# Optimization experiments

Measured on AMD Instinct MI355X. Metric: run time of the kernel, lower is better.

## Reference

```python
import jax, jax.numpy as jnp
import numpy as np

E = 16        # n_experts
N = 4         # n_mhc
D = 512       # d_hidden
D_FFN = int(D * 1.618)  # 828
TOP_PROB = 0.8
MAX_K = 4
SINKHORN_ITERS = 6
EPS = 1e-8


def top_prob_max_k(logits, threshold=TOP_PROB, max_k=MAX_K):
    probs = jax.nn.softmax(logits, axis=-1)
    order = jnp.argsort(-probs, axis=-1)                       # descending sort indices
    sorted_p = jnp.take_along_axis(probs, order, axis=-1)
    cumsum = jnp.cumsum(sorted_p, axis=-1)
    ar = jnp.arange(logits.shape[-1])
    mask = (cumsum - sorted_p < threshold) & (ar < max_k)
    mask = mask.at[..., 0].set(True)
    selected = sorted_p * mask.astype(probs.dtype)
    inv = jnp.argsort(order, axis=-1)                          # inverse permutation == scatter
    return jnp.take_along_axis(selected, inv, axis=-1)


def sinkhorn_knopp(M, n_iters=SINKHORN_ITERS):
    M = jnp.exp(M)
    for _ in range(n_iters):
        M = M / M.sum(axis=-1, keepdims=True)
        M = M / M.sum(axis=-2, keepdims=True)
    return M


def setup_inputs() -> dict:
    key = jax.random.key(0)
    ks = jax.random.split(key, 12)
    nd = N * D
    inp = {
        'stream': jax.random.normal(ks[0], (2, N, 1024, D), dtype=jnp.float32),
        # BatchedMHC params
        'norm_w': jnp.ones((E, nd), dtype=jnp.float32),
        'phi_pre_w': jax.random.normal(ks[1], (E, N, nd), dtype=jnp.float32) * 0.01,
        'phi_post_w': jax.random.normal(ks[2], (E, N, nd), dtype=jnp.float32) * 0.01,
        'phi_res_w': jax.random.normal(ks[3], (E, N * N, nd), dtype=jnp.float32) * 0.01,
        'b_pre': jnp.zeros((E, N), dtype=jnp.float32),
        'b_post': jnp.zeros((E, N), dtype=jnp.float32),
        'b_res': jnp.zeros((E, N, N), dtype=jnp.float32),
        'alpha_pre': jnp.ones((E,), dtype=jnp.float32),
        'alpha_post': jnp.ones((E,), dtype=jnp.float32),
        'alpha_res': jnp.ones((E,), dtype=jnp.float32),
        # SwiGLU expert params
        'swiglu_norm_w': jnp.ones((E, D), dtype=jnp.float32),
        'swiglu_wd_w': jax.random.normal(ks[4], (E, D, D), dtype=jnp.float32) * 0.01,
        'swiglu_wu_w': jax.random.normal(ks[5], (E, D, D), dtype=jnp.float32) * 0.01,
        'swiglu_gate_w': jax.random.normal(ks[6], (E, D_FFN, D), dtype=jnp.float32) * 0.01,
        'swiglu_up_w': jax.random.normal(ks[7], (E, D_FFN, D), dtype=jnp.float32) * 0.01,
        'swiglu_down_w': jax.random.normal(ks[8], (E, D, D_FFN), dtype=jnp.float32) * 0.01,
        # router (nn.Linear without bias): logits = x @ W.T, W: (E, D)
        'router_w': jax.random.normal(ks[9], (E, D), dtype=jnp.float32) * (1.0 / np.sqrt(D)),
    }
    return inp


def reference(stream, norm_w, phi_pre_w, phi_post_w, phi_res_w,
              b_pre, b_post, b_res, alpha_pre, alpha_post, alpha_res,
              swiglu_norm_w, swiglu_wd_w, swiglu_wu_w,
              swiglu_gate_w, swiglu_up_w, swiglu_down_w, router_w):
    B, n, T, d = stream.shape
    nd = n * d

    # ---- routing (eval mode: no gumbel) ----
    route_input = stream.mean(axis=1)                               # (B,T,d)
    router_logits = jnp.einsum('btd,ed->bte', route_input, router_w)
    gate_moe = top_prob_max_k(router_logits)                        # (B,T,E)
    router_probs = jax.nn.softmax(router_logits, axis=-1)
    moe_mask = (gate_moe > 0).astype(router_probs.dtype)
    route_lp = (jnp.maximum(jnp.log(router_probs), -10.0) * moe_mask).sum(-1)  # (B,T)

    # Original gathers active experts (always excluding expert 0) and skips gate==0
    # experts; since gate_e multiplies each expert's output, computing all experts
    # 1..E-1 is mathematically identical. K = E-1.
    sl = slice(1, E)

    # ---- BatchedMHC ----
    x = stream.transpose(0, 2, 1, 3).reshape(B, T, nd)              # (B,T,nd)
    rms = jax.lax.rsqrt(jnp.mean(x * x, axis=-1, keepdims=True) + EPS)
    xn = x * rms                                                    # (B,T,nd)
    # fold per-expert norm weight into the phi projections (avoids K*B*T*nd tensor)
    phi_pre_eff = phi_pre_w[sl] * norm_w[sl, None, :]               # (K,n,nd)
    phi_post_eff = phi_post_w[sl] * norm_w[sl, None, :]
    phi_res_eff = phi_res_w[sl] * norm_w[sl, None, :]               # (K,n*n,nd)

    H_pre = jax.nn.sigmoid(alpha_pre[sl, None, None, None]
                           * jnp.einsum('btd,knd->kbtn', xn, phi_pre_eff)
                           + b_pre[sl, None, None, :])              # (K,B,T,n)
    H_post = 2.0 * jax.nn.sigmoid(alpha_post[sl, None, None, None]
                                  * jnp.einsum('btd,knd->kbtn', xn, phi_post_eff)
                                  + b_post[sl, None, None, :])      # (K,B,T,n)
    res_e = jnp.einsum('btd,knd->kbtn', xn, phi_res_eff)
    K = E - 1
    H_res_raw = (alpha_res[sl].reshape(K, 1, 1, 1, 1)
                 * res_e.reshape(K, B, T, n, n)
                 + b_res[sl, None, None, :, :])
    H_res = sinkhorn_knopp(H_res_raw)                               # (K,B,T,n,n)

    # ---- per-expert SwiGLU ----
    h_e = jnp.einsum('kbtn,bntd->kbtd', H_pre, stream)              # (K,B,T,d)
    rms2 = jax.lax.rsqrt(jnp.mean(h_e * h_e, axis=-1, keepdims=True) + EPS)
    h = h_e * rms2 * swiglu_norm_w[sl, None, None, :]

    wd_out = jnp.einsum('kbtd,kod->kbto', h, swiglu_wd_w[sl])
    g = jax.nn.sigmoid(jnp.einsum('kbtd,kod->kbto', jax.nn.silu(wd_out), swiglu_wu_w[sl]))
    gate_out = jnp.einsum('kbtd,kod->kbto', h, swiglu_gate_w[sl])   # (K,B,T,d_ffn)
    up_out = jnp.einsum('kbtd,kod->kbto', h, swiglu_up_w[sl])
    out_e = g * jnp.einsum('kbtf,kof->kbto', jax.nn.silu(gate_out) * up_out,
                           swiglu_down_w[sl])                        # (K,B,T,d)

    # ---- combine ----
    gate_4d = gate_moe[:, :, 1:].transpose(2, 0, 1)[:, :, None, :, None]  # (K,B,1,T,1)
    res = jnp.einsum('kbtij,bjtd->kbitd', H_res, stream)            # (K,B,n,T,d)
    post = jnp.einsum('kbtn,kbtd->kbntd', H_post, out_e)            # (K,B,n,T,d)
    stream_update = (gate_4d * (res + post)).sum(axis=0)            # (B,n,T,d)

    return stream_update, gate_moe, route_lp
```

## Files before the change

### kernel.cpp

```cpp
#include <hip/hip_runtime.h>
#include <hip/hip_bf16.h>
#include <math.h>

typedef __attribute__((ext_vector_type(8))) short short8;
typedef __attribute__((ext_vector_type(4))) float floatx4;

#define T_LEN 1024
#define D_H 512
#define ND 2048
#define KEXP 15
#define DFFN 828
#define DFFN_P 896
#define BT_TOT 2048
#define PHI_ROWS 360
#define PHI_ROWS_P 384
#define PAIR_CAP 9216

#define WD_OFF   0
#define WU_OFF   262144
#define GATE_OFF 524288
#define UP_OFF   983040
#define DOWN_OFF 1441792
#define EXPW     1900544

#define BK 32

__device__ __forceinline__ float sigmoidf_(float x) { return 1.f / (1.f + expf(-x)); }
__device__ __forceinline__ unsigned short bf16b_(float x) {
    __hip_bfloat16 h = __float2bfloat16(x);
    return *reinterpret_cast<unsigned short*>(&h);
}

__device__ __forceinline__ void gload16(const __hip_bfloat16* g, unsigned short* l) {
    __builtin_amdgcn_global_load_lds(
        (const __attribute__((address_space(1))) void*)(uintptr_t)g,
        (__attribute__((address_space(3))) void*)(unsigned int)(uintptr_t)l,
        16, 0, 0);
}

__global__ __launch_bounds__(64) void router_kernel(
    const float* __restrict__ stream, const float* __restrict__ rw,
    float* __restrict__ gate_out, float* __restrict__ lp_out,
    int* __restrict__ cnt, int* __restrict__ list, int* __restrict__ pos)
{
    int bt = blockIdx.x; int b = bt >> 10; int t = bt & 1023;
    int lane = threadIdx.x;
    float ri[8];
#pragma unroll
    for (int w = 0; w < 8; ++w) {
        int d = lane + w * 64;
        float s = 0.f;
#pragma unroll
        for (int n = 0; n < 4; ++n)
            s += stream[(((size_t)b * 4 + n) * T_LEN + t) * D_H + d];
        ri[w] = 0.25f * s;
    }
    float logits[16];
    for (int e = 0; e < 16; ++e) {
        float p = 0.f;
#pragma unroll
        for (int w = 0; w < 8; ++w) p += ri[w] * rw[e * D_H + lane + w * 64];
#pragma unroll
        for (int off = 32; off; off >>= 1) p += __shfl_xor(p, off, 64);
        logits[e] = p;
    }
    float mx = logits[0];
    for (int e = 1; e < 16; ++e) mx = fmaxf(mx, logits[e]);
    float pr[16]; float sum = 0.f;
    for (int e = 0; e < 16; ++e) { pr[e] = expf(logits[e] - mx); sum += pr[e]; }
    float inv = 1.f / sum;
    for (int e = 0; e < 16; ++e) pr[e] *= inv;

    float gate[16]; bool taken[16];
    for (int e = 0; e < 16; ++e) { gate[e] = 0.f; taken[e] = false; }
    float prefix = 0.f;
    for (int rank = 0; rank < 4; ++rank) {
        int best = -1; float bp = -1.f;
        for (int e = 0; e < 16; ++e)
            if (!taken[e] && pr[e] > bp) { bp = pr[e]; best = e; }
        taken[best] = true;
        bool sel = (rank == 0) || (prefix < 0.8f);
        if (sel) gate[best] = bp;
        prefix += bp;
        if (!sel) break;
    }
    float lp = 0.f;
    for (int e = 0; e < 16; ++e)
        if (gate[e] > 0.f) lp += fmaxf(logf(pr[e]), -10.f);
    if (lane < 16) gate_out[(size_t)bt * 16 + lane] = gate[lane];
    if (lane == 0) lp_out[bt] = lp;
    if (lane >= 1 && lane < 16 && gate[lane] > 0.f) {
        int k = lane - 1;
        int p = atomicAdd(&cnt[k], 1);
        list[k * BT_TOT + p] = bt;
        pos[k * BT_TOT + bt] = p;
    }
}

__global__ void scan_kernel(const int* __restrict__ cnt, int* __restrict__ offs) {
    if (threadIdx.x == 0) {
        int a = 0;
        for (int k = 0; k < KEXP; ++k) { offs[k] = a; a += (cnt[k] + 63) & ~63; }
        offs[KEXP] = a;
    }
}

__global__ __launch_bounds__(256) void xn_kernel(
    const float* __restrict__ stream, __hip_bfloat16* __restrict__ xn)
{
    int bt = blockIdx.x; int b = bt >> 10; int t = bt & 1023;
    int tid = threadIdx.x;
    float v[8]; float ss = 0.f;
#pragma unroll
    for (int w = 0; w < 8; ++w) {
        int j = tid + w * 256;
        int n = j >> 9, d = j & 511;
        float x = stream[(((size_t)b * 4 + n) * T_LEN + t) * D_H + d];
        v[w] = x; ss += x * x;
    }
#pragma unroll
    for (int off = 32; off; off >>= 1) ss += __shfl_down(ss, off, 64);
    __shared__ float red[4];
    int wave = tid >> 6, lane = tid & 63;
    if (lane == 0) red[wave] = ss;
    __syncthreads();
    float tot = red[0] + red[1] + red[2] + red[3];
    float r = rsqrtf(tot / (float)ND + 1e-8f);
#pragma unroll
    for (int w = 0; w < 8; ++w)
        xn[(size_t)bt * ND + tid + w * 256] = __float2bfloat16(v[w] * r);
}

__global__ __launch_bounds__(256) void cvt_phi_kernel(
    const float* __restrict__ norm_w, const float* __restrict__ phi_pre,
    const float* __restrict__ phi_post, const float* __restrict__ phi_res,
    __hip_bfloat16* __restrict__ phi_all)
{
    int idx = blockIdx.x * 256 + threadIdx.x;
    int row = idx >> 11, col = idx & 2047;
    float v = 0.f;
    if (row < PHI_ROWS) {
        int k = row / 24, j = row - k * 24, e = k + 1;
        float nw = norm_w[(size_t)e * ND + col];
        float p;
        if (j < 4)      p = phi_pre[((size_t)e * 4 + j) * ND + col];
        else if (j < 8) p = phi_post[((size_t)e * 4 + (j - 4)) * ND + col];
        else            p = phi_res[((size_t)e * 16 + (j - 8)) * ND + col];
        v = p * nw;
    }
    phi_all[idx] = __float2bfloat16(v);
}

__global__ __launch_bounds__(256) void cvt_all_kernel(
    const float* __restrict__ wd, const float* __restrict__ wu,
    const float* __restrict__ gate, const float* __restrict__ up,
    const float* __restrict__ down, __hip_bfloat16* __restrict__ wbuf, int e0)
{
    int z = blockIdx.z;
    int type = blockIdx.y;
    int g = blockIdx.x * 256 + threadIdx.x;
    int e = e0 + z;
    __hip_bfloat16* dstb = wbuf + (size_t)z * EXPW;
    float4 v = make_float4(0.f, 0.f, 0.f, 0.f);
    size_t didx;
    if (type <= 1) {
        if (g >= 65536) return;
        didx = (type == 0 ? WD_OFF : WU_OFF) + (size_t)g * 4;
        const float* src = (type == 0 ? wd : wu) + (size_t)e * 262144;
        v = *(const float4*)(src + (size_t)g * 4);
    } else if (type <= 3) {
        if (g >= 114688) return;
        size_t idx4 = (size_t)g * 4;
        didx = (type == 2 ? GATE_OFF : UP_OFF) + idx4;
        if (idx4 < (size_t)DFFN * 512) {
            const float* src = (type == 2 ? gate : up) + (size_t)e * DFFN * 512;
            v = *(const float4*)(src + idx4);
        }
    } else {
        if (g >= 114688) return;
        int r = g / 224, gc = g - r * 224;
        didx = DOWN_OFF + (size_t)g * 4;
        if (gc < 207)
            v = *(const float4*)(down + (size_t)e * 512 * DFFN + (size_t)r * DFFN + gc * 4);
    }
    ushort4 o;
    o.x = bf16b_(v.x); o.y = bf16b_(v.y); o.z = bf16b_(v.z); o.w = bf16b_(v.w);
    *(ushort4*)((unsigned short*)dstb + didx) = o;
}

#define LDSS 40
__global__ __launch_bounds__(256) void gemm_dense(
    const __hip_bfloat16* __restrict__ A, const __hip_bfloat16* __restrict__ W,
    float* __restrict__ Cf, int Ka, int Oc, int kLen, int kzStride)
{
    __shared__ __align__(16) unsigned short As[128 * LDSS];
    __shared__ __align__(16) unsigned short Ws[128 * LDSS];
    int z = blockIdx.z;
    int bo = blockIdx.x * 128;
    int bm = blockIdx.y * 128;
    int kbeg = z * kzStride;
    int tid = threadIdx.x;
    int wid = tid >> 6, lane = tid & 63;
    int quad = lane >> 4, lr = lane & 15;
    int wm = (wid & 1) * 64, wn = (wid >> 1) * 64;
    int srow = tid >> 2;
    int schk = (tid & 3) * 8;

    floatx4 acc[4][4];
#pragma unroll
    for (int i = 0; i < 4; ++i)
#pragma unroll
        for (int j = 0; j < 4; ++j) { floatx4 zv = {0.f, 0.f, 0.f, 0.f}; acc[i][j] = zv; }

    for (int k0 = kbeg; k0 < kbeg + kLen; k0 += BK) {
        float4 a0 = *(const float4*)(A + (size_t)(bm + srow) * Ka + k0 + schk);
        float4 a1 = *(const float4*)(A + (size_t)(bm + srow + 64) * Ka + k0 + schk);
        float4 w0 = *(const float4*)(W + (size_t)(bo + srow) * Ka + k0 + schk);
        float4 w1 = *(const float4*)(W + (size_t)(bo + srow + 64) * Ka + k0 + schk);
        __syncthreads();
        *(float4*)&As[srow * LDSS + schk] = a0;
        *(float4*)&As[(srow + 64) * LDSS + schk] = a1;
        *(float4*)&Ws[srow * LDSS + schk] = w0;
        *(float4*)&Ws[(srow + 64) * LDSS + schk] = w1;
        __syncthreads();
        short8 af[4], bf[4];
#pragma unroll
        for (int mi = 0; mi < 4; ++mi)
            af[mi] = *(const short8*)&As[(wm + mi * 16 + lr) * LDSS + quad * 8];
#pragma unroll
        for (int ni = 0; ni < 4; ++ni)
            bf[ni] = *(const short8*)&Ws[(wn + ni * 16 + lr) * LDSS + quad * 8];
#pragma unroll
        for (int mi = 0; mi < 4; ++mi)
#pragma unroll
            for (int ni = 0; ni < 4; ++ni)
                acc[mi][ni] = __builtin_amdgcn_mfma_f32_16x16x32_bf16(
                    af[mi], bf[ni], acc[mi][ni], 0, 0, 0);
    }
#pragma unroll
    for (int mi = 0; mi < 4; ++mi) {
        int row0 = bm + wm + mi * 16 + quad * 4;
#pragma unroll
        for (int ni = 0; ni < 4; ++ni) {
            int col = bo + wn + ni * 16 + lr;
#pragma unroll
            for (int r = 0; r < 4; ++r)
                atomicAdd(&Cf[(size_t)(row0 + r) * Oc + col], acc[mi][ni][r]);
        }
    }
}

__global__ __launch_bounds__(256) void gemm_stage1(
    const __hip_bfloat16* __restrict__ hA, const __hip_bfloat16* __restrict__ wbuf,
    __hip_bfloat16* __restrict__ s1A, __hip_bfloat16* __restrict__ tA,
    const int* __restrict__ cnt, const int* __restrict__ offs, int kg)
{
    __shared__ __align__(16) unsigned short As[64 * 32];
    __shared__ __align__(16) unsigned short Gs[128 * 32];
    __shared__ __align__(16) unsigned short Us[128 * 32];
    int z = blockIdx.z;
    int k = kg + z;
    int bm = blockIdx.y * 64;
    if (bm >= cnt[k]) return;
    int base = offs[k];
    bool dual = (blockIdx.x >= 4);
    int bo = (dual ? (blockIdx.x - 4) : blockIdx.x) * 128;
    const __hip_bfloat16* Ab = hA + (size_t)base * D_H;
    const __hip_bfloat16* W1 = wbuf + (size_t)z * EXPW + (dual ? GATE_OFF : WD_OFF);
    const __hip_bfloat16* W2 = wbuf + (size_t)z * EXPW + UP_OFF;
    int tid = threadIdx.x;
    int wid = tid >> 6, lane = tid & 63;
    int quad = lane >> 4, lr = lane & 15;
    int lrow = lane >> 2, lchk = lane & 3;
    int achk = lchk ^ ((lrow >> 1) & 3);
    int fs = quad ^ ((lr >> 1) & 3);
    int wm = (wid & 1) * 32, wn = (wid >> 1) * 64;

    floatx4 a1[2][4], a2[2][4];
#pragma unroll
    for (int i = 0; i < 2; ++i)
#pragma unroll
        for (int j = 0; j < 4; ++j) {
            floatx4 zv = {0.f, 0.f, 0.f, 0.f};
            a1[i][j] = zv; a2[i][j] = zv;
        }

    int sr0 = wid * 16 + lrow;
    int sr1 = (wid + 4) * 16 + lrow;
    const size_t aoff  = (size_t)(bm + sr0) * D_H + achk * 8;
    const size_t g0off = (size_t)(bo + sr0) * D_H + achk * 8;
    const size_t g1off = (size_t)(bo + sr1) * D_H + achk * 8;

    for (int k0 = 0; k0 < D_H; k0 += BK) {
        __syncthreads();
        gload16(Ab + aoff + k0, As + wid * 512);
        gload16(W1 + g0off + k0, Gs + wid * 512);
        gload16(W1 + g1off + k0, Gs + (wid + 4) * 512);
        if (dual) {
            gload16(W2 + g0off + k0, Us + wid * 512);
            gload16(W2 + g1off + k0, Us + (wid + 4) * 512);
        }
        __syncthreads();
        short8 af[2], bg[4];
#pragma unroll
        for (int mi = 0; mi < 2; ++mi)
            af[mi] = *(const short8*)&As[(wm + mi * 16 + lr) * 32 + fs * 8];
#pragma unroll
        for (int ni = 0; ni < 4; ++ni)
            bg[ni] = *(const short8*)&Gs[(wn + ni * 16 + lr) * 32 + fs * 8];
#pragma unroll
        for (int mi = 0; mi < 2; ++mi)
#pragma unroll
            for (int ni = 0; ni < 4; ++ni)
                a1[mi][ni] = __builtin_amdgcn_mfma_f32_16x16x32_bf16(
                    af[mi], bg[ni], a1[mi][ni], 0, 0, 0);
        if (dual) {
            short8 bu[4];
#pragma unroll
            for (int ni = 0; ni < 4; ++ni)
                bu[ni] = *(const short8*)&Us[(wn + ni * 16 + lr) * 32 + fs * 8];
#pragma unroll
            for (int mi = 0; mi < 2; ++mi)
#pragma unroll
                for (int ni = 0; ni < 4; ++ni)
                    a2[mi][ni] = __builtin_amdgcn_mfma_f32_16x16x32_bf16(
                        af[mi], bu[ni], a2[mi][ni], 0, 0, 0);
        }
    }

#pragma unroll
    for (int mi = 0; mi < 2; ++mi) {
        int row0 = bm + wm + mi * 16 + quad * 4;
#pragma unroll
        for (int ni = 0; ni < 4; ++ni) {
            int col = bo + wn + ni * 16 + lr;
#pragma unroll
            for (int r = 0; r < 4; ++r) {
                float v = a1[mi][ni][r];
                if (dual) {
                    float uu = a2[mi][ni][r];
                    tA[(size_t)(base + row0 + r) * DFFN_P + col] =
                        __float2bfloat16(v * sigmoidf_(v) * uu);
                } else {
                    s1A[(size_t)(base + row0 + r) * D_H + col] =
                        __float2bfloat16(v * sigmoidf_(v));
                }
            }
        }
    }
}

__global__ __launch_bounds__(256) void gemm_final(
    const __hip_bfloat16* __restrict__ s1A, const __hip_bfloat16* __restrict__ tA,
    const __hip_bfloat16* __restrict__ wbuf, __hip_bfloat16* __restrict__ outeA,
    const int* __restrict__ cnt, const int* __restrict__ offs, int kg)
{
    __shared__ __align__(16) unsigned short As[64 * 32];
    __shared__ __align__(16) unsigned short Ws[128 * 32];
    int z = blockIdx.z;
    int k = kg + z;
    int bm = blockIdx.y * 64;
    if (bm >= cnt[k]) return;
    int base = offs[k];
    int bo = blockIdx.x * 128;
    const __hip_bfloat16* A1 = s1A + (size_t)base * D_H;
    const __hip_bfloat16* A2 = tA + (size_t)base * DFFN_P;
    const __hip_bfloat16* Wu = wbuf + (size_t)z * EXPW + WU_OFF;
    const __hip_bfloat16* Wd = wbuf + (size_t)z * EXPW + DOWN_OFF;
    int tid = threadIdx.x;
    int wid = tid >> 6, lane = tid & 63;
    int quad = lane >> 4, lr = lane & 15;
    int lrow = lane >> 2, lchk = lane & 3;
    int achk = lchk ^ ((lrow >> 1) & 3);
    int fs = quad ^ ((lr >> 1) & 3);
    int wm = (wid & 1) * 32, wn = (wid >> 1) * 64;
    int sr0 = wid * 16 + lrow;
    int sr1 = (wid + 4) * 16 + lrow;

    floatx4 accg[2][4], accd[2][4];
#pragma unroll
    for (int i = 0; i < 2; ++i)
#pragma unroll
        for (int j = 0; j < 4; ++j) {
            floatx4 zv = {0.f, 0.f, 0.f, 0.f};
            accg[i][j] = zv; accd[i][j] = zv;
        }

    for (int k0 = 0; k0 < D_H; k0 += BK) {
        __syncthreads();
        gload16(A1 + (size_t)(bm + sr0) * D_H + k0 + achk * 8, As + wid * 512);
        gload16(Wu + (size_t)(bo + sr0) * D_H + k0 + achk * 8, Ws + wid * 512);
        gload16(Wu + (size_t)(bo + sr1) * D_H + k0 + achk * 8, Ws + (wid + 4) * 512);
        __syncthreads();
        short8 af[2], bf[4];
#pragma unroll
        for (int mi = 0; mi < 2; ++mi)
            af[mi] = *(const short8*)&As[(wm + mi * 16 + lr) * 32 + fs * 8];
#pragma unroll
        for (int ni = 0; ni < 4; ++ni)
            bf[ni] = *(const short8*)&Ws[(wn + ni * 16 + lr) * 32 + fs * 8];
#pragma unroll
        for (int mi = 0; mi < 2; ++mi)
#pragma unroll
            for (int ni = 0; ni < 4; ++ni)
                accg[mi][ni] = __builtin_amdgcn_mfma_f32_16x16x32_bf16(
                    af[mi], bf[ni], accg[mi][ni], 0, 0, 0);
    }
    for (int k0 = 0; k0 < DFFN_P; k0 += BK) {
        __syncthreads();
        gload16(A2 + (size_t)(bm + sr0) * DFFN_P + k0 + achk * 8, As + wid * 512);
        gload16(Wd + (size_t)(bo + sr0) * DFFN_P + k0 + achk * 8, Ws + wid * 512);
        gload16(Wd + (size_t)(bo + sr1) * DFFN_P + k0 + achk * 8, Ws + (wid + 4) * 512);
        __syncthreads();
        short8 af[2], bf[4];
#pragma unroll
        for (int mi = 0; mi < 2; ++mi)
            af[mi] = *(const short8*)&As[(wm + mi * 16 + lr) * 32 + fs * 8];
#pragma unroll
        for (int ni = 0; ni < 4; ++ni)
            bf[ni] = *(const short8*)&Ws[(wn + ni * 16 + lr) * 32 + fs * 8];
#pragma unroll
        for (int mi = 0; mi < 2; ++mi)
#pragma unroll
            for (int ni = 0; ni < 4; ++ni)
                accd[mi][ni] = __builtin_amdgcn_mfma_f32_16x16x32_bf16(
                    af[mi], bf[ni], accd[mi][ni], 0, 0, 0);
    }

#pragma unroll
    for (int mi = 0; mi < 2; ++mi) {
        int row0 = bm + wm + mi * 16 + quad * 4;
#pragma unroll
        for (int ni = 0; ni < 4; ++ni) {
            int col = bo + wn + ni * 16 + lr;
#pragma unroll
            for (int r = 0; r < 4; ++r) {
                float g = accg[mi][ni][r];
                float d = accd[mi][ni][r];
                outeA[(size_t)(base + row0 + r) * D_H + col] =
                    __float2bfloat16(sigmoidf_(g) * d);
            }
        }
    }
}

__global__ __launch_bounds__(256) void mhc_post_kernel(
    const float* __restrict__ Cproj,
    const float* __restrict__ b_pre, const float* __restrict__ b_post,
    const float* __restrict__ b_res, const float* __restrict__ a_pre,
    const float* __restrict__ a_post, const float* __restrict__ a_res,
    float* __restrict__ Hpre, float* __restrict__ Hpost, float* __restrict__ Hres)
{
    int gid = blockIdx.x * 256 + threadIdx.x;
    int k = gid >> 11, bt = gid & 2047, e = k + 1;
    const float* s = Cproj + (size_t)bt * PHI_ROWS_P + k * 24;
    float ap = a_pre[e], aq = a_post[e], ar = a_res[e];
#pragma unroll
    for (int n = 0; n < 4; ++n)
        Hpre[((size_t)k * BT_TOT + bt) * 4 + n] = sigmoidf_(ap * s[n] + b_pre[e * 4 + n]);
#pragma unroll
    for (int n = 0; n < 4; ++n)
        Hpost[((size_t)k * BT_TOT + bt) * 4 + n] = 2.f * sigmoidf_(aq * s[4 + n] + b_post[e * 4 + n]);
    float M[16];
#pragma unroll
    for (int i = 0; i < 16; ++i) M[i] = expf(ar * s[8 + i] + b_res[e * 16 + i]);
#pragma unroll
    for (int it = 0; it < 6; ++it) {
#pragma unroll
        for (int i = 0; i < 4; ++i) {
            float iv = 1.f / (M[i*4] + M[i*4+1] + M[i*4+2] + M[i*4+3]);
            M[i*4] *= iv; M[i*4+1] *= iv; M[i*4+2] *= iv; M[i*4+3] *= iv;
        }
#pragma unroll
        for (int j = 0; j < 4; ++j) {
            float iv = 1.f / (M[j] + M[4+j] + M[8+j] + M[12+j]);
            M[j] *= iv; M[4+j] *= iv; M[8+j] *= iv; M[12+j] *= iv;
        }
    }
#pragma unroll
    for (int i = 0; i < 16; ++i) Hres[((size_t)k * BT_TOT + bt) * 16 + i] = M[i];
}

__global__ __launch_bounds__(256) void h_kernel(
    const float* __restrict__ stream, const float* __restrict__ Hpre,
    const float* __restrict__ sw_norm, const int* __restrict__ list,
    const int* __restrict__ counts, const int* __restrict__ offs,
    __hip_bfloat16* __restrict__ hA)
{
    int k = blockIdx.y;
    int i = blockIdx.x;
    if (i >= counts[k]) return;
    int bt = list[k * BT_TOT + i];
    int e = k + 1;
    int b = bt >> 10, t = bt & 1023;
    int tid = threadIdx.x;
    float hp[4];
#pragma unroll
    for (int n = 0; n < 4; ++n) hp[n] = Hpre[((size_t)k * BT_TOT + bt) * 4 + n];
    float he[2]; float ss = 0.f;
#pragma unroll
    for (int w = 0; w < 2; ++w) {
        int d = tid + w * 256;
        float v = 0.f;
#pragma unroll
        for (int n = 0; n < 4; ++n)
            v += hp[n] * stream[(((size_t)b * 4 + n) * T_LEN + t) * D_H + d];
        he[w] = v; ss += v * v;
    }
#pragma unroll
    for (int off = 32; off; off >>= 1) ss += __shfl_down(ss, off, 64);
    __shared__ float red[4];
    int wave = tid >> 6, lane = tid & 63;
    if (lane == 0) red[wave] = ss;
    __syncthreads();
    float tot = red[0] + red[1] + red[2] + red[3];
    float r = rsqrtf(tot / (float)D_H + 1e-8f);
    size_t row = (size_t)(offs[k] + i);
#pragma unroll
    for (int w = 0; w < 2; ++w) {
        int d = tid + w * 256;
        hA[row * D_H + d] = __float2bfloat16(he[w] * r * sw_norm[(size_t)e * D_H + d]);
    }
}

__global__ __launch_bounds__(256) void combine_kernel(
    const float* __restrict__ stream, const __hip_bfloat16* __restrict__ outeA,
    const float* __restrict__ Hpost, const float* __restrict__ Hres,
    const float* __restrict__ gate_all, const int* __restrict__ pos,
    const int* __restrict__ offs, float* __restrict__ out)
{
    int bt = blockIdx.x; int b = bt >> 10; int t = bt & 1023;
    int tid = threadIdx.x;
    float s[2][4], accv[2][4];
#pragma unroll
    for (int w = 0; w < 2; ++w) {
        int d = tid + w * 256;
#pragma unroll
        for (int n = 0; n < 4; ++n) {
            s[w][n] = stream[(((size_t)b * 4 + n) * T_LEN + t) * D_H + d];
            accv[w][n] = 0.f;
        }
    }
    for (int k = 0; k < KEXP; ++k) {
        float gate = gate_all[(size_t)bt * 16 + k + 1];
        if (gate == 0.f) continue;
        size_t row = (size_t)(offs[k] + pos[k * BT_TOT + bt]);
        float hr[16], hp[4];
#pragma unroll
        for (int i = 0; i < 16; ++i) hr[i] = Hres[((size_t)k * BT_TOT + bt) * 16 + i];
#pragma unroll
        for (int i = 0; i < 4; ++i) hp[i] = Hpost[((size_t)k * BT_TOT + bt) * 4 + i];
#pragma unroll
        for (int w = 0; w < 2; ++w) {
            int d = tid + w * 256;
            float oe = __bfloat162float(outeA[row * D_H + d]);
#pragma unroll
            for (int i = 0; i < 4; ++i) {
                float v = hp[i] * oe + hr[i*4+0]*s[w][0] + hr[i*4+1]*s[w][1]
                        + hr[i*4+2]*s[w][2] + hr[i*4+3]*s[w][3];
                accv[w][i] += gate * v;
            }
        }
    }
#pragma unroll
    for (int w = 0; w < 2; ++w) {
        int d = tid + w * 256;
#pragma unroll
        for (int i = 0; i < 4; ++i)
            out[(((size_t)b * 4 + i) * T_LEN + t) * D_H + d] = accv[w][i];
    }
}

extern "C" void kernel_launch(void* const* d_in, const int* in_sizes, int n_in,
                              void* d_out, int out_size, void* d_ws, size_t ws_size,
                              hipStream_t stream) {
    const float* stream_in = (const float*)d_in[0];
    const float* norm_w    = (const float*)d_in[1];
    const float* phi_pre   = (const float*)d_in[2];
    const float* phi_post  = (const float*)d_in[3];
    const float* phi_res   = (const float*)d_in[4];
    const float* b_pre     = (const float*)d_in[5];
    const float* b_post    = (const float*)d_in[6];
    const float* b_res     = (const float*)d_in[7];
    const float* alpha_pre = (const float*)d_in[8];
    const float* alpha_post= (const float*)d_in[9];
    const float* alpha_res = (const float*)d_in[10];
    const float* sw_norm   = (const float*)d_in[11];
    const float* wd_w      = (const float*)d_in[12];
    const float* wu_w      = (const float*)d_in[13];
    const float* gate_w    = (const float*)d_in[14];
    const float* up_w      = (const float*)d_in[15];
    const float* down_w    = (const float*)d_in[16];
    const float* router_w  = (const float*)d_in[17];

    float* out = (float*)d_out;
    const int SU_N = 2 * 4 * T_LEN * D_H;
    float* gate_out = out + SU_N;
    float* lp_out = gate_out + BT_TOT * 16;

    char* p = (char*)d_ws;
    __hip_bfloat16* xn     = (__hip_bfloat16*)p; p += (size_t)BT_TOT * ND * 2;
    __hip_bfloat16* phiall = (__hip_bfloat16*)p; p += (size_t)PHI_ROWS_P * ND * 2;
    float* Cproj = (float*)p; p += (size_t)BT_TOT * PHI_ROWS_P * 4;
    float* Hpre  = (float*)p; p += (size_t)KEXP * BT_TOT * 4 * 4;
    float* Hpost = (float*)p; p += (size_t)KEXP * BT_TOT * 4 * 4;
    float* Hres  = (float*)p; p += (size_t)KEXP * BT_TOT * 16 * 4;
    int* cnt  = (int*)p; p += 256;
    int* offs = (int*)p; p += 256;
    int* list = (int*)p; p += (size_t)KEXP * BT_TOT * 4;
    int* pos  = (int*)p; p += (size_t)KEXP * BT_TOT * 4;
    __hip_bfloat16* hA    = (__hip_bfloat16*)p; p += (size_t)PAIR_CAP * D_H * 2;
    __hip_bfloat16* s1A   = (__hip_bfloat16*)p; p += (size_t)PAIR_CAP * D_H * 2;
    __hip_bfloat16* outeA = (__hip_bfloat16*)p; p += (size_t)PAIR_CAP * D_H * 2;
    __hip_bfloat16* tA    = (__hip_bfloat16*)p; p += (size_t)PAIR_CAP * DFFN_P * 2;
    size_t fixed_bytes = (size_t)(p - (char*)d_ws);
    size_t perW = (size_t)EXPW * 2;
    size_t avail = ws_size > fixed_bytes ? ws_size - fixed_bytes : 0;
    int G = (int)(avail / perW);
    if (G > KEXP) G = KEXP;
    if (G < 1) G = 1;
    __hip_bfloat16* wbuf = (__hip_bfloat16*)p;

    hipMemsetAsync(cnt, 0, 64, stream);
    hipMemsetAsync(Cproj, 0, (size_t)BT_TOT * PHI_ROWS_P * 4, stream);
    router_kernel<<<BT_TOT, 64, 0, stream>>>(
        stream_in, router_w, gate_out, lp_out, cnt, list, pos);
    scan_kernel<<<1, 64, 0, stream>>>(cnt, offs);
    xn_kernel<<<BT_TOT, 256, 0, stream>>>(stream_in, xn);
    cvt_phi_kernel<<<(PHI_ROWS_P * ND) / 256, 256, 0, stream>>>(
        norm_w, phi_pre, phi_post, phi_res, phiall);
    gemm_dense<<<dim3(3, 16, 4), 256, 0, stream>>>(
        xn, phiall, Cproj, ND, PHI_ROWS_P, 512, 512);
    mhc_post_kernel<<<(KEXP * BT_TOT) / 256, 256, 0, stream>>>(
        Cproj, b_pre, b_post, b_res, alpha_pre, alpha_post, alpha_res, Hpre, Hpost, Hres);
    h_kernel<<<dim3(BT_TOT, KEXP), 256, 0, stream>>>(
        stream_in, Hpre, sw_norm, list, cnt, offs, hA);

    for (int kg = 0; kg < KEXP; kg += G) {
        int Gc = (kg + G <= KEXP) ? G : (KEXP - kg);
        int e0 = kg + 1;
        cvt_all_kernel<<<dim3(448, 5, Gc), 256, 0, stream>>>(
            wd_w, wu_w, gate_w, up_w, down_w, wbuf, e0);
        gemm_stage1<<<dim3(11, 32, Gc), 256, 0, stream>>>(
            hA, wbuf, s1A, tA, cnt, offs, kg);
        gemm_final<<<dim3(4, 32, Gc), 256, 0, stream>>>(
            s1A, tA, wbuf, outeA, cnt, offs, kg);
    }

    combine_kernel<<<BT_TOT, 256, 0, stream>>>(
        stream_in, outeA, Hpost, Hres, gate_out, pos, offs, out);
}
```

Baseline: 400.3 us.

## Fuse router into RMS-norm prep, fold MHC post into h_kernel, enlarge expert GEMM M-tile

Merges the router and xn normalization kernels into one prep_kernel that reads the stream once, and moves the per-pair Sinkhorn/sigmoid MHC coefficient computation into h_kernel so the Hpre buffer and the separate mhc_post launch go away. The expert GEMMs switch to 128-row M tiles with 512 threads, halving the number of M blocks and letting each wave load one row slice. Segment padding grows to 128 and the pair capacity is raised to match. In exchange, a single thread does the routing softmax/top-k serially per block, and the Sinkhorn work now runs on one thread inside h_kernel before a block barrier.

```diff
diff --git a/kernel.cpp b/kernel.cpp
--- a/kernel.cpp
+++ b/kernel.cpp
@@ -14,7 +14,7 @@
 #define BT_TOT 2048
 #define PHI_ROWS 360
 #define PHI_ROWS_P 384
-#define PAIR_CAP 9216
+#define PAIR_CAP 10240
 
 #define WD_OFF   0
 #define WU_OFF   262144
@@ -38,78 +38,15 @@
         16, 0, 0);
 }
 
-__global__ __launch_bounds__(64) void router_kernel(
+__global__ __launch_bounds__(256) void prep_kernel(
     const float* __restrict__ stream, const float* __restrict__ rw,
-    float* __restrict__ gate_out, float* __restrict__ lp_out,
-    int* __restrict__ cnt, int* __restrict__ list, int* __restrict__ pos)
-{
-    int bt = blockIdx.x; int b = bt >> 10; int t = bt & 1023;
-    int lane = threadIdx.x;
-    float ri[8];
-#pragma unroll
-    for (int w = 0; w < 8; ++w) {
-        int d = lane + w * 64;
-        float s = 0.f;
-#pragma unroll
-        for (int n = 0; n < 4; ++n)
-            s += stream[(((size_t)b * 4 + n) * T_LEN + t) * D_H + d];
-        ri[w] = 0.25f * s;
-    }
-    float logits[16];
-    for (int e = 0; e < 16; ++e) {
-        float p = 0.f;
-#pragma unroll
-        for (int w = 0; w < 8; ++w) p += ri[w] * rw[e * D_H + lane + w * 64];
-#pragma unroll
-        for (int off = 32; off; off >>= 1) p += __shfl_xor(p, off, 64);
-        logits[e] = p;
-    }
-    float mx = logits[0];
-    for (int e = 1; e < 16; ++e) mx = fmaxf(mx, logits[e]);
-    float pr[16]; float sum = 0.f;
-    for (int e = 0; e < 16; ++e) { pr[e] = expf(logits[e] - mx); sum += pr[e]; }
-    float inv = 1.f / sum;
-    for (int e = 0; e < 16; ++e) pr[e] *= inv;
-
-    float gate[16]; bool taken[16];
-    for (int e = 0; e < 16; ++e) { gate[e] = 0.f; taken[e] = false; }
-    float prefix = 0.f;
-    for (int rank = 0; rank < 4; ++rank) {
-        int best = -1; float bp = -1.f;
-        for (int e = 0; e < 16; ++e)
-            if (!taken[e] && pr[e] > bp) { bp = pr[e]; best = e; }
-        taken[best] = true;
-        bool sel = (rank == 0) || (prefix < 0.8f);
-        if (sel) gate[best] = bp;
-        prefix += bp;
-        if (!sel) break;
-    }
-    float lp = 0.f;
-    for (int e = 0; e < 16; ++e)
-        if (gate[e] > 0.f) lp += fmaxf(logf(pr[e]), -10.f);
-    if (lane < 16) gate_out[(size_t)bt * 16 + lane] = gate[lane];
-    if (lane == 0) lp_out[bt] = lp;
-    if (lane >= 1 && lane < 16 && gate[lane] > 0.f) {
-        int k = lane - 1;
-        int p = atomicAdd(&cnt[k], 1);
-        list[k * BT_TOT + p] = bt;
-        pos[k * BT_TOT + bt] = p;
-    }
-}
-
-__global__ void scan_kernel(const int* __restrict__ cnt, int* __restrict__ offs) {
-    if (threadIdx.x == 0) {
-        int a = 0;
-        for (int k = 0; k < KEXP; ++k) { offs[k] = a; a += (cnt[k] + 63) & ~63; }
-        offs[KEXP] = a;
-    }
-}
-
-__global__ __launch_bounds__(256) void xn_kernel(
-    const float* __restrict__ stream, __hip_bfloat16* __restrict__ xn)
+    __hip_bfloat16* __restrict__ xn, float* __restrict__ gate_out,
+    float* __restrict__ lp_out, int* __restrict__ cnt,
+    int* __restrict__ list, int* __restrict__ pos)
 {
     int bt = blockIdx.x; int b = bt >> 10; int t = bt & 1023;
     int tid = threadIdx.x;
+    int wave = tid >> 6, lane = tid & 63;
     float v[8]; float ss = 0.f;
 #pragma unroll
     for (int w = 0; w < 8; ++w) {
@@ -118,17 +55,71 @@
         float x = stream[(((size_t)b * 4 + n) * T_LEN + t) * D_H + d];
         v[w] = x; ss += x * x;
     }
+    float m0 = 0.25f * (v[0] + v[2] + v[4] + v[6]);
+    float m1 = 0.25f * (v[1] + v[3] + v[5] + v[7]);
+    __shared__ float redE[4][16];
+    __shared__ float logit_s[16];
+    for (int e = 0; e < 16; ++e) {
+        float p = m0 * rw[e * D_H + tid] + m1 * rw[e * D_H + tid + 256];
+#pragma unroll
+        for (int off = 32; off; off >>= 1) p += __shfl_xor(p, off, 64);
+        if (lane == 0) redE[wave][e] = p;
+    }
 #pragma unroll
     for (int off = 32; off; off >>= 1) ss += __shfl_down(ss, off, 64);
-    __shared__ float red[4];
-    int wave = tid >> 6, lane = tid & 63;
-    if (lane == 0) red[wave] = ss;
+    __shared__ float redS[4];
+    if (lane == 0) redS[wave] = ss;
     __syncthreads();
-    float tot = red[0] + red[1] + red[2] + red[3];
+    if (tid < 16) logit_s[tid] = redE[0][tid] + redE[1][tid] + redE[2][tid] + redE[3][tid];
+    __syncthreads();
+    if (tid == 0) {
+        float pr[16];
+        float mx = logit_s[0];
+        for (int e = 1; e < 16; ++e) mx = fmaxf(mx, logit_s[e]);
+        float sum = 0.f;
+        for (int e = 0; e < 16; ++e) { pr[e] = expf(logit_s[e] - mx); sum += pr[e]; }
+        float inv = 1.f / sum;
+        for (int e = 0; e < 16; ++e) pr[e] *= inv;
+        float gate[16]; bool taken[16];
+        for (int e = 0; e < 16; ++e) { gate[e] = 0.f; taken[e] = false; }
+        float prefix = 0.f;
+        for (int rank = 0; rank < 4; ++rank) {
+            int best = -1; float bp = -1.f;
+            for (int e = 0; e < 16; ++e)
+                if (!taken[e] && pr[e] > bp) { bp = pr[e]; best = e; }
+            taken[best] = true;
+            bool sel = (rank == 0) || (prefix < 0.8f);
+            if (sel) gate[best] = bp;
+            prefix += bp;
+            if (!sel) break;
+        }
+        float lp = 0.f;
+        for (int e = 0; e < 16; ++e) {
+            gate_out[(size_t)bt * 16 + e] = gate[e];
+            if (gate[e] > 0.f) lp += fmaxf(logf(pr[e]), -10.f);
+        }
+        lp_out[bt] = lp;
+        for (int e = 1; e < 16; ++e)
+            if (gate[e] > 0.f) {
+                int k = e - 1;
+                int p = atomicAdd(&cnt[k], 1);
+                list[k * BT_TOT + p] = bt;
+                pos[k * BT_TOT + bt] = p;
+            }
+    }
+    float tot = redS[0] + redS[1] + redS[2] + redS[3];
     float r = rsqrtf(tot / (float)ND + 1e-8f);
 #pragma unroll
     for (int w = 0; w < 8; ++w)
         xn[(size_t)bt * ND + tid + w * 256] = __float2bfloat16(v[w] * r);
+}
+
+__global__ void scan_kernel(const int* __restrict__ cnt, int* __restrict__ offs) {
+    if (threadIdx.x == 0) {
+        int a = 0;
+        for (int k = 0; k < KEXP; ++k) { offs[k] = a; a += (cnt[k] + 127) & ~127; }
+        offs[KEXP] = a;
+    }
 }
 
 __global__ __launch_bounds__(256) void cvt_phi_kernel(
@@ -250,17 +241,17 @@
     }
 }
 
-__global__ __launch_bounds__(256) void gemm_stage1(
+__global__ __launch_bounds__(512) void gemm_stage1(
     const __hip_bfloat16* __restrict__ hA, const __hip_bfloat16* __restrict__ wbuf,
     __hip_bfloat16* __restrict__ s1A, __hip_bfloat16* __restrict__ tA,
     const int* __restrict__ cnt, const int* __restrict__ offs, int kg)
 {
-    __shared__ __align__(16) unsigned short As[64 * 32];
+    __shared__ __align__(16) unsigned short As[128 * 32];
     __shared__ __align__(16) unsigned short Gs[128 * 32];
     __shared__ __align__(16) unsigned short Us[128 * 32];
     int z = blockIdx.z;
     int k = kg + z;
-    int bm = blockIdx.y * 64;
+    int bm = blockIdx.y * 128;
     if (bm >= cnt[k]) return;
     int base = offs[k];
     bool dual = (blockIdx.x >= 4);
@@ -274,7 +265,9 @@
     int lrow = lane >> 2, lchk = lane & 3;
     int achk = lchk ^ ((lrow >> 1) & 3);
     int fs = quad ^ ((lr >> 1) & 3);
-    int wm = (wid & 1) * 32, wn = (wid >> 1) * 64;
+    int wm = (wid & 3) * 32, wn = (wid >> 2) * 64;
+    int srow = wid * 16 + lrow;
+    int ldsb = wid * 512;
 
     floatx4 a1[2][4], a2[2][4];
 #pragma unroll
@@ -285,21 +278,14 @@
             a1[i][j] = zv; a2[i][j] = zv;
         }
 
-    int sr0 = wid * 16 + lrow;
-    int sr1 = (wid + 4) * 16 + lrow;
-    const size_t aoff  = (size_t)(bm + sr0) * D_H + achk * 8;
-    const size_t g0off = (size_t)(bo + sr0) * D_H + achk * 8;
-    const size_t g1off = (size_t)(bo + sr1) * D_H + achk * 8;
+    const size_t aoff = (size_t)(bm + srow) * D_H + achk * 8;
+    const size_t woff = (size_t)(bo + srow) * D_H + achk * 8;
 
     for (int k0 = 0; k0 < D_H; k0 += BK) {
         __syncthreads();
-        gload16(Ab + aoff + k0, As + wid * 512);
-        gload16(W1 + g0off + k0, Gs + wid * 512);
-        gload16(W1 + g1off + k0, Gs + (wid + 4) * 512);
-        if (dual) {
-            gload16(W2 + g0off + k0, Us + wid * 512);
-            gload16(W2 + g1off + k0, Us + (wid + 4) * 512);
-        }
+        gload16(Ab + aoff + k0, As + ldsb);
+        gload16(W1 + woff + k0, Gs + ldsb);
+        if (dual) gload16(W2 + woff + k0, Us + ldsb);
         __syncthreads();
         short8 af[2], bg[4];
 #pragma unroll
@@ -350,16 +336,16 @@
     }
 }
 
-__global__ __launch_bounds__(256) void gemm_final(
+__global__ __launch_bounds__(512) void gemm_final(
     const __hip_bfloat16* __restrict__ s1A, const __hip_bfloat16* __restrict__ tA,
     const __hip_bfloat16* __restrict__ wbuf, __hip_bfloat16* __restrict__ outeA,
     const int* __restrict__ cnt, const int* __restrict__ offs, int kg)
 {
-    __shared__ __align__(16) unsigned short As[64 * 32];
+    __shared__ __align__(16) unsigned short As[128 * 32];
     __shared__ __align__(16) unsigned short Ws[128 * 32];
     int z = blockIdx.z;
     int k = kg + z;
-    int bm = blockIdx.y * 64;
+    int bm = blockIdx.y * 128;
     if (bm >= cnt[k]) return;
     int base = offs[k];
     int bo = blockIdx.x * 128;
@@ -373,9 +359,9 @@
     int lrow = lane >> 2, lchk = lane & 3;
     int achk = lchk ^ ((lrow >> 1) & 3);
     int fs = quad ^ ((lr >> 1) & 3);
-    int wm = (wid & 1) * 32, wn = (wid >> 1) * 64;
-    int sr0 = wid * 16 + lrow;
-    int sr1 = (wid + 4) * 16 + lrow;
+    int wm = (wid & 3) * 32, wn = (wid >> 2) * 64;
+    int srow = wid * 16 + lrow;
+    int ldsb = wid * 512;
 
     floatx4 accg[2][4], accd[2][4];
 #pragma unroll
@@ -388,9 +374,8 @@
 
     for (int k0 = 0; k0 < D_H; k0 += BK) {
         __syncthreads();
-        gload16(A1 + (size_t)(bm + sr0) * D_H + k0 + achk * 8, As + wid * 512);
-        gload16(Wu + (size_t)(bo + sr0) * D_H + k0 + achk * 8, Ws + wid * 512);
-        gload16(Wu + (size_t)(bo + sr1) * D_H + k0 + achk * 8, Ws + (wid + 4) * 512);
+        gload16(A1 + (size_t)(bm + srow) * D_H + k0 + achk * 8, As + ldsb);
+        gload16(Wu + (size_t)(bo + srow) * D_H + k0 + achk * 8, Ws + ldsb);
         __syncthreads();
         short8 af[2], bf[4];
 #pragma unroll
@@ -408,9 +393,8 @@
     }
     for (int k0 = 0; k0 < DFFN_P; k0 += BK) {
         __syncthreads();
-        gload16(A2 + (size_t)(bm + sr0) * DFFN_P + k0 + achk * 8, As + wid * 512);
-        gload16(Wd + (size_t)(bo + sr0) * DFFN_P + k0 + achk * 8, Ws + wid * 512);
-        gload16(Wd + (size_t)(bo + sr1) * DFFN_P + k0 + achk * 8, Ws + (wid + 4) * 512);
+        gload16(A2 + (size_t)(bm + srow) * DFFN_P + k0 + achk * 8, As + ldsb);
+        gload16(Wd + (size_t)(bo + srow) * DFFN_P + k0 + achk * 8, Ws + ldsb);
         __syncthreads();
         short8 af[2], bf[4];
 #pragma unroll
@@ -444,48 +428,15 @@
     }
 }
 
-__global__ __launch_bounds__(256) void mhc_post_kernel(
-    const float* __restrict__ Cproj,
+__global__ __launch_bounds__(256) void h_kernel(
+    const float* __restrict__ stream, const float* __restrict__ Cproj,
     const float* __restrict__ b_pre, const float* __restrict__ b_post,
     const float* __restrict__ b_res, const float* __restrict__ a_pre,
     const float* __restrict__ a_post, const float* __restrict__ a_res,
-    float* __restrict__ Hpre, float* __restrict__ Hpost, float* __restrict__ Hres)
-{
-    int gid = blockIdx.x * 256 + threadIdx.x;
-    int k = gid >> 11, bt = gid & 2047, e = k + 1;
-    const float* s = Cproj + (size_t)bt * PHI_ROWS_P + k * 24;
-    float ap = a_pre[e], aq = a_post[e], ar = a_res[e];
-#pragma unroll
-    for (int n = 0; n < 4; ++n)
-        Hpre[((size_t)k * BT_TOT + bt) * 4 + n] = sigmoidf_(ap * s[n] + b_pre[e * 4 + n]);
-#pragma unroll
-    for (int n = 0; n < 4; ++n)
-        Hpost[((size_t)k * BT_TOT + bt) * 4 + n] = 2.f * sigmoidf_(aq * s[4 + n] + b_post[e * 4 + n]);
-    float M[16];
-#pragma unroll
-    for (int i = 0; i < 16; ++i) M[i] = expf(ar * s[8 + i] + b_res[e * 16 + i]);
-#pragma unroll
-    for (int it = 0; it < 6; ++it) {
-#pragma unroll
-        for (int i = 0; i < 4; ++i) {
-            float iv = 1.f / (M[i*4] + M[i*4+1] + M[i*4+2] + M[i*4+3]);
-            M[i*4] *= iv; M[i*4+1] *= iv; M[i*4+2] *= iv; M[i*4+3] *= iv;
-        }
-#pragma unroll
-        for (int j = 0; j < 4; ++j) {
-            float iv = 1.f / (M[j] + M[4+j] + M[8+j] + M[12+j]);
-            M[j] *= iv; M[4+j] *= iv; M[8+j] *= iv; M[12+j] *= iv;
-        }
-    }
-#pragma unroll
-    for (int i = 0; i < 16; ++i) Hres[((size_t)k * BT_TOT + bt) * 16 + i] = M[i];
-}
-
-__global__ __launch_bounds__(256) void h_kernel(
-    const float* __restrict__ stream, const float* __restrict__ Hpre,
     const float* __restrict__ sw_norm, const int* __restrict__ list,
     const int* __restrict__ counts, const int* __restrict__ offs,
-    __hip_bfloat16* __restrict__ hA)
+    __hip_bfloat16* __restrict__ hA, float* __restrict__ Hpost,
+    float* __restrict__ Hres)
 {
     int k = blockIdx.y;
     int i = blockIdx.x;
@@ -494,9 +445,40 @@
     int e = k + 1;
     int b = bt >> 10, t = bt & 1023;
     int tid = threadIdx.x;
+    __shared__ float HpreS[4];
+    if (tid == 0) {
+        const float* s = Cproj + (size_t)bt * PHI_ROWS_P + k * 24;
+        float ap = a_pre[e], aq = a_post[e], ar = a_res[e];
+#pragma unroll
+        for (int n = 0; n < 4; ++n)
+            HpreS[n] = sigmoidf_(ap * s[n] + b_pre[e * 4 + n]);
+#pragma unroll
+        for (int n = 0; n < 4; ++n)
+            Hpost[((size_t)k * BT_TOT + bt) * 4 + n] =
+                2.f * sigmoidf_(aq * s[4 + n] + b_post[e * 4 + n]);
+        float M[16];
+#pragma unroll
+        for (int j = 0; j < 16; ++j) M[j] = expf(ar * s[8 + j] + b_res[e * 16 + j]);
+#pragma unroll
+        for (int it = 0; it < 6; ++it) {
+#pragma unroll
+            for (int r = 0; r < 4; ++r) {
+                float iv = 1.f / (M[r*4] + M[r*4+1] + M[r*4+2] + M[r*4+3]);
+                M[r*4] *= iv; M[r*4+1] *= iv; M[r*4+2] *= iv; M[r*4+3] *= iv;
+            }
+#pragma unroll
+            for (int c = 0; c < 4; ++c) {
+                float iv = 1.f / (M[c] + M[4+c] + M[8+c] + M[12+c]);
+                M[c] *= iv; M[4+c] *= iv; M[8+c] *= iv; M[12+c] *= iv;
+            }
+        }
+#pragma unroll
+        for (int j = 0; j < 16; ++j) Hres[((size_t)k * BT_TOT + bt) * 16 + j] = M[j];
+    }
+    __syncthreads();
     float hp[4];
 #pragma unroll
-    for (int n = 0; n < 4; ++n) hp[n] = Hpre[((size_t)k * BT_TOT + bt) * 4 + n];
+    for (int n = 0; n < 4; ++n) hp[n] = HpreS[n];
     float he[2]; float ss = 0.f;
 #pragma unroll
     for (int w = 0; w < 2; ++w) {
@@ -602,7 +584,6 @@
     __hip_bfloat16* xn     = (__hip_bfloat16*)p; p += (size_t)BT_TOT * ND * 2;
     __hip_bfloat16* phiall = (__hip_bfloat16*)p; p += (size_t)PHI_ROWS_P * ND * 2;
     float* Cproj = (float*)p; p += (size_t)BT_TOT * PHI_ROWS_P * 4;
-    float* Hpre  = (float*)p; p += (size_t)KEXP * BT_TOT * 4 * 4;
     float* Hpost = (float*)p; p += (size_t)KEXP * BT_TOT * 4 * 4;
     float* Hres  = (float*)p; p += (size_t)KEXP * BT_TOT * 16 * 4;
     int* cnt  = (int*)p; p += 256;
@@ -623,27 +604,25 @@
 
     hipMemsetAsync(cnt, 0, 64, stream);
     hipMemsetAsync(Cproj, 0, (size_t)BT_TOT * PHI_ROWS_P * 4, stream);
-    router_kernel<<<BT_TOT, 64, 0, stream>>>(
-        stream_in, router_w, gate_out, lp_out, cnt, list, pos);
+    prep_kernel<<<BT_TOT, 256, 0, stream>>>(
+        stream_in, router_w, xn, gate_out, lp_out, cnt, list, pos);
     scan_kernel<<<1, 64, 0, stream>>>(cnt, offs);
-    xn_kernel<<<BT_TOT, 256, 0, stream>>>(stream_in, xn);
     cvt_phi_kernel<<<(PHI_ROWS_P * ND) / 256, 256, 0, stream>>>(
         norm_w, phi_pre, phi_post, phi_res, phiall);
     gemm_dense<<<dim3(3, 16, 4), 256, 0, stream>>>(
         xn, phiall, Cproj, ND, PHI_ROWS_P, 512, 512);
-    mhc_post_kernel<<<(KEXP * BT_TOT) / 256, 256, 0, stream>>>(
-        Cproj, b_pre, b_post, b_res, alpha_pre, alpha_post, alpha_res, Hpre, Hpost, Hres);
     h_kernel<<<dim3(BT_TOT, KEXP), 256, 0, stream>>>(
-        stream_in, Hpre, sw_norm, list, cnt, offs, hA);
+        stream_in, Cproj, b_pre, b_post, b_res, alpha_pre, alpha_post, alpha_res,
+        sw_norm, list, cnt, offs, hA, Hpost, Hres);
 
     for (int kg = 0; kg < KEXP; kg += G) {
         int Gc = (kg + G <= KEXP) ? G : (KEXP - kg);
         int e0 = kg + 1;
         cvt_all_kernel<<<dim3(448, 5, Gc), 256, 0, stream>>>(
             wd_w, wu_w, gate_w, up_w, down_w, wbuf, e0);
-        gemm_stage1<<<dim3(11, 32, Gc), 256, 0, stream>>>(
+        gemm_stage1<<<dim3(11, 16, Gc), 512, 0, stream>>>(
             hA, wbuf, s1A, tA, cnt, offs, kg);
-        gemm_final<<<dim3(4, 32, Gc), 256, 0, stream>>>(
+        gemm_final<<<dim3(4, 16, Gc), 512, 0, stream>>>(
             s1A, tA, wbuf, outeA, cnt, offs, kg);
     }
 
```

Measured after the change: 451.9 us. 1.13x slower.
